# Optimization experiments

Hardware: AMD Instinct MI355X
Metric: run time of the kernel (lower is better)

Reference implementation:

```python
import jax, jax.numpy as jnp
import numpy as np
from math import ceil

B, N, C_IN, H, EDIM = 64, 512, 128, 128, 5
EPG = 16 * N          # edges per graph
E = B * EPG           # 524288 edges total
K1 = ceil(0.5 * N)    # 256 clusters after pool 1
K2 = ceil(0.5 * K1)   # 128 clusters after pool 2
EPS = 1e-15


def dense_mincut_pool(x, adj, s, mask=None):
    # x: [B,n,F], adj: [B,n,n], s: [B,n,k]
    s = jax.nn.softmax(s, axis=-1)
    if mask is not None:
        m = mask[..., None].astype(x.dtype)
        x = x * m
        s = s * m
    out = jnp.einsum('bnk,bnf->bkf', s, x)
    out_adj = jnp.einsum('bnk,bnm,bml->bkl', s, adj, s)
    mincut_num = jnp.trace(out_adj, axis1=-2, axis2=-1)
    d_flat = adj.sum(-1)                                   # degrees [B,n]
    mincut_den = jnp.trace(jnp.einsum('bnk,bn,bnl->bkl', s, d_flat, s), axis1=-2, axis2=-1)
    mincut_loss = jnp.mean(-(mincut_num / mincut_den))
    k = s.shape[-1]
    ss = jnp.einsum('bnk,bnl->bkl', s, s)
    ss_norm = jnp.linalg.norm(ss, axis=(-1, -2), keepdims=True)
    i_s = jnp.eye(k, dtype=x.dtype)
    ortho_loss = jnp.mean(jnp.linalg.norm(ss / ss_norm - i_s / np.sqrt(k), axis=(-1, -2)))
    out_adj = out_adj * (1.0 - i_s)                        # zero diagonal
    d = jnp.sqrt(out_adj.sum(-1))[..., None] + EPS
    out_adj = out_adj / d / jnp.swapaxes(d, -1, -2)
    return out, out_adj, mincut_loss, ortho_loss


def setup_inputs() -> dict:
    key = jax.random.key(0)
    ks = iter(jax.random.split(key, 40))
    NT = B * N
    x = jax.random.normal(next(ks), (NT, C_IN), jnp.float32)
    # within-graph random edges; nodes are sorted by graph (batch = repeat)
    offs = jnp.repeat(jnp.arange(B, dtype=jnp.int32) * N, EPG)
    src = jax.random.randint(next(ks), (E,), 0, N, jnp.int32) + offs
    dst = jax.random.randint(next(ks), (E,), 0, N, jnp.int32) + offs
    edge_index = jnp.stack([src, dst])
    edge_attr = jax.random.normal(next(ks), (E, EDIM), jnp.float32)
    batch = jnp.repeat(jnp.arange(B, dtype=jnp.int32), N)

    def W(shape):
        return jax.random.normal(next(ks), shape, jnp.float32) * 0.05

    inp = dict(x=x, edge_index=edge_index, edge_attr=edge_attr, batch=batch,
               bn_gamma=jnp.ones((C_IN,), jnp.float32), bn_beta=jnp.zeros((C_IN,), jnp.float32),
               Wq=W((C_IN, H)), bq=W((H,)), Wk=W((C_IN, H)), bk=W((H,)),
               Wv=W((C_IN, H)), bv=W((H,)), We=W((EDIM, H)),
               Wskip=W((C_IN, H)), bskip=W((H,)),
               W_mlp1=W((H, K1)), b_mlp1=W((K1,)),
               W2_rel=W((H, H)), b2_rel=W((H,)), W2_root=W((H, H)),
               W_mlp2=W((H, K2)), b_mlp2=W((K2,)),
               W3_rel=W((H, H)), b3_rel=W((H,)), W3_root=W((H, H)),
               W_lin1=W((H, H)), b_lin1=W((H,)),
               W_ro=W((H, 1)), b_ro=W((1,)))
    return inp


def reference(x, edge_index, edge_attr, batch, bn_gamma, bn_beta,
              Wq, bq, Wk, bk, Wv, bv, We, Wskip, bskip,
              W_mlp1, b_mlp1, W2_rel, b2_rel, W2_root,
              W_mlp2, b_mlp2, W3_rel, b3_rel, W3_root,
              W_lin1, b_lin1, W_ro, b_ro):
    NT = x.shape[0]
    # BatchNorm1d (training-mode batch statistics, biased var, eps=1e-5)
    mu = x.mean(0)
    var = x.var(0)
    xh = (x - mu) / jnp.sqrt(var + 1e-5) * bn_gamma + bn_beta

    # TransformerConv (heads=1, concat=True, root_weight=True, edge_dim=5)
    src, dst = edge_index[0], edge_index[1]
    q = xh @ Wq + bq
    k_ = xh @ Wk + bk
    v = xh @ Wv + bv
    e = edge_attr @ We                       # lin_edge has no bias
    kj = k_[src] + e
    vj = v[src] + e
    logits = (q[dst] * kj).sum(-1) / np.sqrt(H)
    m = jax.ops.segment_max(logits, dst, num_segments=NT)
    a = jnp.exp(logits - m[dst])
    denom = jax.ops.segment_sum(a, dst, num_segments=NT)
    alpha = a / denom[dst]
    agg = jax.ops.segment_sum(alpha[:, None] * vj, dst, num_segments=NT)
    h = jax.nn.relu(agg + xh @ Wskip + bskip)

    # to_dense_batch: equal-size graphs sorted by batch -> reshape
    xd = h.reshape(B, N, H)
    mask = jnp.ones((B, N), bool)
    # to_dense_adj: scatter-add edge indicators (duplicates accumulate)
    adj = jnp.zeros((B, N, N), jnp.float32).at[batch[src], src % N, dst % N].add(1.0)

    s = xd @ W_mlp1 + b_mlp1
    xd, adj, mc1, o1 = dense_mincut_pool(xd, adj, s, mask)
    # DenseGraphConv: lin_rel(adj @ x) + lin_root(x)
    xd = jax.nn.relu((adj @ xd) @ W2_rel + b2_rel + xd @ W2_root)
    s = xd @ W_mlp2 + b_mlp2
    xd, adj, mc2, o2 = dense_mincut_pool(xd, adj, s)
    xd = (adj @ xd) @ W3_rel + b3_rel + xd @ W3_root
    g = xd.mean(1)
    g = jax.nn.relu(g @ W_lin1 + b_lin1)
    return jax.nn.sigmoid(g @ W_ro + b_ro).squeeze(-1)   # [B]
```

## Files before the change

### kernel.cpp

```cpp
#include <hip/hip_runtime.h>
#include <math.h>

#define BGRAPH 64
#define NNODE  512
#define NTOT   32768
#define CIN    128
#define HDIM   128
#define EDIM_  5
#define EDGES  524288
#define K1C    256
#define K2C    128

using f32x4 = __attribute__((ext_vector_type(4))) float;
using s16x8 = __attribute__((ext_vector_type(8))) short;

__device__ __forceinline__ short f2bf(float f) {
    union { float f; unsigned u; } v; v.f = f;
    unsigned r = v.u + 0x7fffu + ((v.u >> 16) & 1u);
    return (short)(r >> 16);
}
__device__ __forceinline__ float bf2f(short s) {
    union { unsigned u; float f; } v; v.u = ((unsigned)(unsigned short)s) << 16;
    return v.f;
}

__global__ __launch_bounds__(256) void prep_kernel(const float* __restrict__ x,
                                                   float* __restrict__ psum,
                                                   float* __restrict__ psq,
                                                   const float* __restrict__ Wq, const float* __restrict__ Wk,
                                                   const float* __restrict__ Wv, const float* __restrict__ Ws,
                                                   const float* __restrict__ bq, const float* __restrict__ bk,
                                                   const float* __restrict__ bv, const float* __restrict__ bs,
                                                   float* __restrict__ W4, float* __restrict__ bias4,
                                                   const int* __restrict__ ei,
                                                   int* __restrict__ deg_src,
                                                   int* __restrict__ deg_dst) {
    __shared__ float ss[128], sq[128];
    int tid = threadIdx.x, bid = blockIdx.x;
    if (bid < 256) {
        long idx0 = (long)bid * 256 + tid;
        float4 s = {0.f, 0.f, 0.f, 0.f}, q = {0.f, 0.f, 0.f, 0.f};
#pragma unroll
        for (int it = 0; it < 16; ++it) {
            float4 v = *(const float4*)(x + (idx0 + (long)it * 65536) * 4);
            s.x += v.x; s.y += v.y; s.z += v.z; s.w += v.w;
            q.x += v.x * v.x; q.y += v.y * v.y; q.z += v.z * v.z; q.w += v.w * v.w;
        }
        if (tid < 128) { ss[tid] = 0.f; sq[tid] = 0.f; }
        __syncthreads();
        int c0 = (tid & 31) * 4;
        atomicAdd(&ss[c0 + 0], s.x); atomicAdd(&ss[c0 + 1], s.y);
        atomicAdd(&ss[c0 + 2], s.z); atomicAdd(&ss[c0 + 3], s.w);
        atomicAdd(&sq[c0 + 0], q.x); atomicAdd(&sq[c0 + 1], q.y);
        atomicAdd(&sq[c0 + 2], q.z); atomicAdd(&sq[c0 + 3], q.w);
        __syncthreads();
        if (tid < 128) {
            psum[bid * 128 + tid] = ss[tid];
            psq[bid * 128 + tid]  = sq[tid];
        }
    } else if (bid < 512) {
        int i = (bid - 256) * 256 + tid;
        if (i < 128 * 512) {
            int k = i / 512, j = i % 512;
            float v;
            if (j < 128)      v = Wq[k * 128 + j];
            else if (j < 256) v = Wk[k * 128 + (j - 128)];
            else if (j < 384) v = Wv[k * 128 + (j - 256)];
            else              v = Ws[k * 128 + (j - 384)];
            W4[i] = v;
        }
        if (i < 512) {
            float v;
            if (i < 128)      v = bq[i];
            else if (i < 256) v = bk[i - 128];
            else if (i < 384) v = bv[i - 256];
            else              v = bs[i - 384];
            bias4[i] = v;
        }
    } else {
        int e = (bid - 512) * 256 + tid;
        if (e < EDGES) {
            atomicAdd(&deg_src[ei[e]], 1);
            atomicAdd(&deg_dst[ei[EDGES + e]], 1);
        }
    }
}

__global__ __launch_bounds__(1024) void scan2fin_kernel(const int* __restrict__ deg_src,
                                                        int* __restrict__ rp_src, int* __restrict__ cur_src,
                                                        const int* __restrict__ deg_dst,
                                                        int* __restrict__ rp_dst, int* __restrict__ cur_dst,
                                                        const float* __restrict__ psum,
                                                        const float* __restrict__ psq,
                                                        const float* __restrict__ gamma,
                                                        const float* __restrict__ beta,
                                                        float* __restrict__ scale,
                                                        float* __restrict__ shift) {
    __shared__ int part[1024];
    int tid = threadIdx.x;
    if (blockIdx.x == 2) {
        if (tid < 128) {
            int c = tid;
            float s = 0.f, q = 0.f;
            for (int b = 0; b < 256; ++b) { s += psum[b * 128 + c]; q += psq[b * 128 + c]; }
            float mu  = s / (float)NTOT;
            float var = q / (float)NTOT - mu * mu;
            float rstd = rsqrtf(var + 1e-5f);
            float sc = gamma[c] * rstd;
            scale[c] = sc;
            shift[c] = beta[c] - mu * sc;
        }
        return;
    }
    const int* deg = blockIdx.x ? deg_dst : deg_src;
    int* rowptr    = blockIdx.x ? rp_dst  : rp_src;
    int* cursor    = blockIdx.x ? cur_dst : cur_src;
    int base = tid * 32;
    int s = 0;
    for (int i = 0; i < 32; ++i) s += deg[base + i];
    part[tid] = s;
    __syncthreads();
    for (int off = 1; off < 1024; off <<= 1) {
        int v = part[tid];
        int add = (tid >= off) ? part[tid - off] : 0;
        __syncthreads();
        part[tid] = v + add;
        __syncthreads();
    }
    int run = (tid == 0) ? 0 : part[tid - 1];
    for (int i = 0; i < 32; ++i) {
        rowptr[base + i] = run;
        cursor[base + i] = run;
        run += deg[base + i];
    }
}

__global__ __launch_bounds__(256) void scatter_kernel(const int* __restrict__ ei,
                                                      int* __restrict__ cur_src, int* __restrict__ cur_dst,
                                                      int* __restrict__ eid_src, int* __restrict__ eid_dst) {
    int e = blockIdx.x * 256 + threadIdx.x;
    if (e < EDGES) {
        int s = ei[e], d = ei[EDGES + e];
        eid_src[atomicAdd(&cur_src[s], 1)] = e;
        eid_dst[atomicAdd(&cur_dst[d], 1)] = e;
    }
}

template <int TILE, bool TRANS_A, bool AFFINE, bool ANORM, bool ROWSUM, bool RELU,
          bool DUAL, bool OBF16, bool AU8, bool BBF16, bool ATRBF16, bool ABF16>
__global__ __launch_bounds__(256) void mgemm(const void* __restrict__ Av,
                                             const void* __restrict__ Bv,
                                             const void* __restrict__ A2v,
                                             const void* __restrict__ B2v,
                                             int Ksplit,
                                             const float* __restrict__ bias,
                                             void* __restrict__ Cv,
                                             const float* __restrict__ scale,
                                             const float* __restrict__ shift,
                                             int M, int Nc, int K,
                                             int lda, int ldb, int ldc,
                                             long sA, long sB, long sC) {
    __shared__ __align__(16) short As[TILE * 40];
    __shared__ __align__(16) short Bs[TILE * 40];
    __shared__ float dvl[ANORM ? 256 : 1];
    constexpr int ASZ = AU8 ? 1 : ((ATRBF16 || ABF16) ? 2 : 4);
    constexpr int BSZ = BBF16 ? 2 : 4;
    const char* Abase = (const char*)Av + (long)blockIdx.z * sA * ASZ;
    const char* Bbase = (const char*)Bv + (long)blockIdx.z * sB * BSZ;
    float* C = (float*)Cv + (OBF16 ? 0 : (long)blockIdx.z * sC);
    short* Cs = (short*)Cv + (OBF16 ? (long)blockIdx.z * sC : 0);
    const int m0 = blockIdx.y * TILE, n0 = blockIdx.x * TILE;
    const int tid = threadIdx.x;
    const int lane16 = tid & 15;
    const int quad = (tid & 63) >> 4;
    const int wrow = (tid >> 6) >> 1, wcol = (tid >> 6) & 1;
    constexpr int WT = TILE / 32;

    if (ANORM) {
        for (int i = tid; i < K; i += 256)
            dvl[i] = 1.f / (sqrtf(scale[(long)blockIdx.z * lda + i]) + 1e-15f);
        __syncthreads();
    }

    f32x4 acc[WT][WT] = {};

    for (int k0 = 0; k0 < K; k0 += 32) {
        const char* Au = Abase; const char* Bu = Bbase; int ku = k0;
        if (DUAL && k0 >= Ksplit) { Au = (const char*)A2v; Bu = (const char*)B2v; ku = k0 - Ksplit; }

        if (!TRANS_A) {
#pragma unroll
            for (int p = 0; p < TILE / 32; ++p) {
                int idx = tid + p * 256;
                int row = idx >> 3, c4 = idx & 7;
                short4 o;
                if (AU8) {
                    unsigned u = *(const unsigned*)((const unsigned char*)Au +
                                                    (long)(m0 + row) * lda + ku + c4 * 4);
                    o = make_short4(f2bf((float)(u & 255u)), f2bf((float)((u >> 8) & 255u)),
                                    f2bf((float)((u >> 16) & 255u)), f2bf((float)((u >> 24) & 255u)));
                } else if (ABF16) {
                    o = *(const short4*)((const short*)Au + (long)(m0 + row) * lda + ku + c4 * 4);
                } else {
                    float4 v = *(const float4*)((const float*)Au + (long)(m0 + row) * lda + ku + c4 * 4);
                    if (AFFINE) {
                        int k = ku + c4 * 4;
                        v.x = v.x * scale[k] + shift[k];
                        v.y = v.y * scale[k + 1] + shift[k + 1];
                        v.z = v.z * scale[k + 2] + shift[k + 2];
                        v.w = v.w * scale[k + 3] + shift[k + 3];
                    }
                    if (ANORM) {
                        int k = ku + c4 * 4;
                        int grow = m0 + row;
                        float dr = dvl[grow];
                        v.x = (grow == k + 0) ? 0.f : v.x * dr * dvl[k + 0];
                        v.y = (grow == k + 1) ? 0.f : v.y * dr * dvl[k + 1];
                        v.z = (grow == k + 2) ? 0.f : v.z * dr * dvl[k + 2];
                        v.w = (grow == k + 3) ? 0.f : v.w * dr * dvl[k + 3];
                    }
                    o = make_short4(f2bf(v.x), f2bf(v.y), f2bf(v.z), f2bf(v.w));
                }
                *(short4*)&As[row * 40 + c4 * 4] = o;
            }
        } else {
            if (TILE == 128 || tid < 128) {
                int c4 = tid >> 3, g = tid & 7;
                short* d = &As[(c4 * 4) * 40 + g * 4];
                if (ATRBF16) {
                    const short* src = (const short*)Au + (long)(ku + g * 4) * lda + m0 + c4 * 4;
                    short4 r0 = *(const short4*)(src);
                    short4 r1 = *(const short4*)(src + lda);
                    short4 r2 = *(const short4*)(src + 2 * lda);
                    short4 r3 = *(const short4*)(src + 3 * lda);
                    *(short4*)(d + 0 * 40) = make_short4(r0.x, r1.x, r2.x, r3.x);
                    *(short4*)(d + 1 * 40) = make_short4(r0.y, r1.y, r2.y, r3.y);
                    *(short4*)(d + 2 * 40) = make_short4(r0.z, r1.z, r2.z, r3.z);
                    *(short4*)(d + 3 * 40) = make_short4(r0.w, r1.w, r2.w, r3.w);
                } else {
                    const float* src = (const float*)Au + (long)(ku + g * 4) * lda + m0 + c4 * 4;
                    float4 r0 = *(const float4*)(src);
                    float4 r1 = *(const float4*)(src + lda);
                    float4 r2 = *(const float4*)(src + 2 * lda);
                    float4 r3 = *(const float4*)(src + 3 * lda);
                    *(short4*)(d + 0 * 40) = make_short4(f2bf(r0.x), f2bf(r1.x), f2bf(r2.x), f2bf(r3.x));
                    *(short4*)(d + 1 * 40) = make_short4(f2bf(r0.y), f2bf(r1.y), f2bf(r2.y), f2bf(r3.y));
                    *(short4*)(d + 2 * 40) = make_short4(f2bf(r0.z), f2bf(r1.z), f2bf(r2.z), f2bf(r3.z));
                    *(short4*)(d + 3 * 40) = make_short4(f2bf(r0.w), f2bf(r1.w), f2bf(r2.w), f2bf(r3.w));
                }
            }
        }
        if (TILE == 128 || tid < 128) {
            int c4 = tid >> 3, g = tid & 7;
            short* d = &Bs[(c4 * 4) * 40 + g * 4];
            if (BBF16) {
                const short* src = (const short*)Bu + (long)(ku + g * 4) * ldb + n0 + c4 * 4;
                short4 r0 = *(const short4*)(src);
                short4 r1 = *(const short4*)(src + ldb);
                short4 r2 = *(const short4*)(src + 2 * ldb);
                short4 r3 = *(const short4*)(src + 3 * ldb);
                *(short4*)(d + 0 * 40) = make_short4(r0.x, r1.x, r2.x, r3.x);
                *(short4*)(d + 1 * 40) = make_short4(r0.y, r1.y, r2.y, r3.y);
                *(short4*)(d + 2 * 40) = make_short4(r0.z, r1.z, r2.z, r3.z);
                *(short4*)(d + 3 * 40) = make_short4(r0.w, r1.w, r2.w, r3.w);
            } else {
                const float* src = (const float*)Bu + (long)(ku + g * 4) * ldb + n0 + c4 * 4;
                float4 r0 = *(const float4*)(src);
                float4 r1 = *(const float4*)(src + ldb);
                float4 r2 = *(const float4*)(src + 2 * ldb);
                float4 r3 = *(const float4*)(src + 3 * ldb);
                *(short4*)(d + 0 * 40) = make_short4(f2bf(r0.x), f2bf(r1.x), f2bf(r2.x), f2bf(r3.x));
                *(short4*)(d + 1 * 40) = make_short4(f2bf(r0.y), f2bf(r1.y), f2bf(r2.y), f2bf(r3.y));
                *(short4*)(d + 2 * 40) = make_short4(f2bf(r0.z), f2bf(r1.z), f2bf(r2.z), f2bf(r3.z));
                *(short4*)(d + 3 * 40) = make_short4(f2bf(r0.w), f2bf(r1.w), f2bf(r2.w), f2bf(r3.w));
            }
        }
        __syncthreads();

        s16x8 af[WT], bf[WT];
#pragma unroll
        for (int t = 0; t < WT; ++t) {
            af[t] = *(const s16x8*)&As[(wrow * (TILE / 2) + t * 16 + lane16) * 40 + quad * 8];
            bf[t] = *(const s16x8*)&Bs[(wcol * (TILE / 2) + t * 16 + lane16) * 40 + quad * 8];
        }
#pragma unroll
        for (int i = 0; i < WT; ++i)
#pragma unroll
            for (int j = 0; j < WT; ++j)
                acc[i][j] = __builtin_amdgcn_mfma_f32_16x16x32_bf16(af[i], bf[j], acc[i][j], 0, 0, 0);
        __syncthreads();
    }

#pragma unroll
    for (int i = 0; i < WT; ++i) {
        int gm = m0 + wrow * (TILE / 2) + i * 16 + quad * 4;
#pragma unroll
        for (int j = 0; j < WT; ++j) {
            int gn = n0 + wcol * (TILE / 2) + j * 16 + lane16;
            float bv = bias ? bias[gn] : 0.f;
#pragma unroll
            for (int r = 0; r < 4; ++r) {
                float val = acc[i][j][r] + bv;
                if (RELU) val = fmaxf(val, 0.f);
                if (OBF16) Cs[(long)(gm + r) * ldc + gn] = f2bf(val);
                else       C[(long)(gm + r) * ldc + gn] = val;
            }
        }
    }

    if (ROWSUM) {
        float* rlA = (float*)As;
        float* rlB = (float*)Bs;
#pragma unroll
        for (int i = 0; i < WT; ++i) {
#pragma unroll
            for (int r = 0; r < 4; ++r) {
                int gm = m0 + wrow * (TILE / 2) + i * 16 + quad * 4 + r;
                float p = 0.f;
#pragma unroll
                for (int j = 0; j < WT; ++j) {
                    int gn = n0 + wcol * (TILE / 2) + j * 16 + lane16;
                    p += (gn == gm) ? 0.f : acc[i][j][r];
                }
#pragma unroll
                for (int off = 1; off < 16; off <<= 1) p += __shfl_xor(p, off);
                if (lane16 == 0) {
                    int rl = wrow * (TILE / 2) + i * 16 + quad * 4 + r;
                    (wcol ? rlB : rlA)[rl] = p;
                }
            }
        }
        __syncthreads();
        float* rout = (float*)shift;
        for (int t = tid; t < TILE; t += 256)
            atomicAdd(&rout[(long)blockIdx.z * M + m0 + t], rlA[t] + rlB[t]);
    }
}

template <int KADJ, bool RELU, bool OBF16>
__global__ __launch_bounds__(256) void fused_gc_kernel(const float* __restrict__ adj,
                                                       const float* __restrict__ rowsum,
                                                       const float* __restrict__ xp,
                                                       const float* __restrict__ Wrel,
                                                       const float* __restrict__ brel,
                                                       const float* __restrict__ Wroot,
                                                       void* __restrict__ Outv) {
    __shared__ __align__(16) short As[64 * 40];
    __shared__ __align__(16) short Bs[128 * 40];
    __shared__ __align__(16) short Tl[64][136];
    __shared__ float dvl[KADJ];
    const int z = blockIdx.y;
    const int m0 = blockIdx.x * 64;
    const int tid = threadIdx.x;
    const int lane16 = tid & 15;
    const int quad = (tid & 63) >> 4;
    const int wrow = (tid >> 6) >> 1, wcol = (tid >> 6) & 1;
    const float* adjz = adj + (long)z * KADJ * KADJ;
    const float* xpz  = xp + (long)z * KADJ * 128;

    for (int i = tid; i < KADJ; i += 256)
        dvl[i] = 1.f / (sqrtf(rowsum[(long)z * KADJ + i]) + 1e-15f);
    __syncthreads();

    f32x4 acc[2][4] = {};
    for (int k0 = 0; k0 < KADJ; k0 += 32) {
#pragma unroll
        for (int p = 0; p < 2; ++p) {
            int idx = tid + p * 256;
            int row = idx >> 3, c4 = idx & 7;
            int grow = m0 + row, k = k0 + c4 * 4;
            float4 v = *(const float4*)(adjz + (long)grow * KADJ + k);
            float dr = dvl[grow];
            v.x = (grow == k + 0) ? 0.f : v.x * dr * dvl[k + 0];
            v.y = (grow == k + 1) ? 0.f : v.y * dr * dvl[k + 1];
            v.z = (grow == k + 2) ? 0.f : v.z * dr * dvl[k + 2];
            v.w = (grow == k + 3) ? 0.f : v.w * dr * dvl[k + 3];
            *(short4*)&As[row * 40 + c4 * 4] =
                make_short4(f2bf(v.x), f2bf(v.y), f2bf(v.z), f2bf(v.w));
        }
        {
            int c4 = tid >> 3, g = tid & 7;
            short* d = &Bs[(c4 * 4) * 40 + g * 4];
            const float* src = xpz + (long)(k0 + g * 4) * 128 + c4 * 4;
            float4 r0 = *(const float4*)(src);
            float4 r1 = *(const float4*)(src + 128);
            float4 r2 = *(const float4*)(src + 256);
            float4 r3 = *(const float4*)(src + 384);
            *(short4*)(d + 0 * 40) = make_short4(f2bf(r0.x), f2bf(r1.x), f2bf(r2.x), f2bf(r3.x));
            *(short4*)(d + 1 * 40) = make_short4(f2bf(r0.y), f2bf(r1.y), f2bf(r2.y), f2bf(r3.y));
            *(short4*)(d + 2 * 40) = make_short4(f2bf(r0.z), f2bf(r1.z), f2bf(r2.z), f2bf(r3.z));
            *(short4*)(d + 3 * 40) = make_short4(f2bf(r0.w), f2bf(r1.w), f2bf(r2.w), f2bf(r3.w));
        }
        __syncthreads();
        s16x8 af[2], bf[4];
#pragma unroll
        for (int t = 0; t < 2; ++t)
            af[t] = *(const s16x8*)&As[(wrow * 32 + t * 16 + lane16) * 40 + quad * 8];
#pragma unroll
        for (int j = 0; j < 4; ++j)
            bf[j] = *(const s16x8*)&Bs[(wcol * 64 + j * 16 + lane16) * 40 + quad * 8];
#pragma unroll
        for (int t = 0; t < 2; ++t)
#pragma unroll
            for (int j = 0; j < 4; ++j)
                acc[t][j] = __builtin_amdgcn_mfma_f32_16x16x32_bf16(af[t], bf[j], acc[t][j], 0, 0, 0);
        __syncthreads();
    }
#pragma unroll
    for (int t = 0; t < 2; ++t)
#pragma unroll
        for (int j = 0; j < 4; ++j)
#pragma unroll
            for (int r = 0; r < 4; ++r)
                Tl[wrow * 32 + t * 16 + quad * 4 + r][wcol * 64 + j * 16 + lane16] =
                    f2bf(acc[t][j][r]);
    __syncthreads();

    f32x4 acc2[2][4] = {};
    for (int k0 = 0; k0 < 256; k0 += 32) {
        const bool useXp = (k0 >= 128);
        const float* Wsrc = useXp ? (Wroot + (long)(k0 - 128) * 128)
                                  : (Wrel + (long)k0 * 128);
        {
            int c4 = tid >> 3, g = tid & 7;
            short* d = &Bs[(c4 * 4) * 40 + g * 4];
            const float* src = Wsrc + (long)(g * 4) * 128 + c4 * 4;
            float4 r0 = *(const float4*)(src);
            float4 r1 = *(const float4*)(src + 128);
            float4 r2 = *(const float4*)(src + 256);
            float4 r3 = *(const float4*)(src + 384);
            *(short4*)(d + 0 * 40) = make_short4(f2bf(r0.x), f2bf(r1.x), f2bf(r2.x), f2bf(r3.x));
            *(short4*)(d + 1 * 40) = make_short4(f2bf(r0.y), f2bf(r1.y), f2bf(r2.y), f2bf(r3.y));
            *(short4*)(d + 2 * 40) = make_short4(f2bf(r0.z), f2bf(r1.z), f2bf(r2.z), f2bf(r3.z));
            *(short4*)(d + 3 * 40) = make_short4(f2bf(r0.w), f2bf(r1.w), f2bf(r2.w), f2bf(r3.w));
        }
        if (useXp) {
#pragma unroll
            for (int p = 0; p < 2; ++p) {
                int idx = tid + p * 256;
                int row = idx >> 3, c4 = idx & 7;
                float4 v = *(const float4*)(xpz + (long)(m0 + row) * 128 + (k0 - 128) + c4 * 4);
                *(short4*)&As[row * 40 + c4 * 4] =
                    make_short4(f2bf(v.x), f2bf(v.y), f2bf(v.z), f2bf(v.w));
            }
        }
        __syncthreads();
        s16x8 af[2], bf[4];
#pragma unroll
        for (int t = 0; t < 2; ++t) {
            int ar = wrow * 32 + t * 16 + lane16;
            af[t] = useXp ? *(const s16x8*)&As[ar * 40 + quad * 8]
                          : *(const s16x8*)&Tl[ar][k0 + quad * 8];
        }
#pragma unroll
        for (int j = 0; j < 4; ++j)
            bf[j] = *(const s16x8*)&Bs[(wcol * 64 + j * 16 + lane16) * 40 + quad * 8];
#pragma unroll
        for (int t = 0; t < 2; ++t)
#pragma unroll
            for (int j = 0; j < 4; ++j)
                acc2[t][j] = __builtin_amdgcn_mfma_f32_16x16x32_bf16(af[t], bf[j], acc2[t][j], 0, 0, 0);
        __syncthreads();
    }

    float* Of = (float*)Outv;
    short* Ob = (short*)Outv;
#pragma unroll
    for (int t = 0; t < 2; ++t) {
#pragma unroll
        for (int j = 0; j < 4; ++j) {
            int gcol = wcol * 64 + j * 16 + lane16;
            float bv = brel[gcol];
#pragma unroll
            for (int r = 0; r < 4; ++r) {
                int grow = m0 + wrow * 32 + t * 16 + quad * 4 + r;
                float val = acc2[t][j][r] + bv;
                if (RELU) val = fmaxf(val, 0.f);
                long oi = ((long)z * KADJ + grow) * 128 + gcol;
                if (OBF16) Ob[oi] = f2bf(val);
                else       Of[oi] = val;
            }
        }
    }
}

template <int NC>
__global__ __launch_bounds__(256) void mlp_softmax_kernel(const short* __restrict__ A,
                                                          const float* __restrict__ W,
                                                          const float* __restrict__ bias,
                                                          short* __restrict__ Out) {
    __shared__ __align__(16) short As[64 * 40];
    __shared__ __align__(16) short Ws[NC * 40];
    const int tid = threadIdx.x;
    const int lane16 = tid & 15;
    const int quad = (tid & 63) >> 4;
    const int wv = tid >> 6;
    const int m0 = blockIdx.x * 64;
    constexpr int NT = NC / 16;

    f32x4 acc[NT] = {};

    for (int k0 = 0; k0 < 128; k0 += 32) {
        {
            int row = tid >> 2, g = tid & 3;
            *(s16x8*)&As[row * 40 + g * 8] =
                *(const s16x8*)(A + (long)(m0 + row) * 128 + k0 + g * 8);
        }
#pragma unroll
        for (int p = 0; p < NC / 128; ++p) {
            int c4 = tid >> 3, g = tid & 7;
            int n0 = p * 128 + c4 * 4;
            short* d = &Ws[n0 * 40 + g * 4];
            const float* src = W + (long)(k0 + g * 4) * NC + n0;
            float4 r0 = *(const float4*)(src);
            float4 r1 = *(const float4*)(src + NC);
            float4 r2 = *(const float4*)(src + 2 * NC);
            float4 r3 = *(const float4*)(src + 3 * NC);
            *(short4*)(d + 0 * 40) = make_short4(f2bf(r0.x), f2bf(r1.x), f2bf(r2.x), f2bf(r3.x));
            *(short4*)(d + 1 * 40) = make_short4(f2bf(r0.y), f2bf(r1.y), f2bf(r2.y), f2bf(r3.y));
            *(short4*)(d + 2 * 40) = make_short4(f2bf(r0.z), f2bf(r1.z), f2bf(r2.z), f2bf(r3.z));
            *(short4*)(d + 3 * 40) = make_short4(f2bf(r0.w), f2bf(r1.w), f2bf(r2.w), f2bf(r3.w));
        }
        __syncthreads();

        s16x8 af = *(const s16x8*)&As[(wv * 16 + lane16) * 40 + quad * 8];
#pragma unroll
        for (int t = 0; t < NT; ++t) {
            s16x8 bf = *(const s16x8*)&Ws[(t * 16 + lane16) * 40 + quad * 8];
            acc[t] = __builtin_amdgcn_mfma_f32_16x16x32_bf16(af, bf, acc[t], 0, 0, 0);
        }
        __syncthreads();
    }

    float mx[4] = {-INFINITY, -INFINITY, -INFINITY, -INFINITY};
#pragma unroll
    for (int t = 0; t < NT; ++t) {
        float bv = bias[t * 16 + lane16];
#pragma unroll
        for (int r = 0; r < 4; ++r) {
            float x = bf2f(f2bf(acc[t][r] + bv));
            acc[t][r] = x;
            mx[r] = fmaxf(mx[r], x);
        }
    }
#pragma unroll
    for (int off = 8; off; off >>= 1)
#pragma unroll
        for (int r = 0; r < 4; ++r) mx[r] = fmaxf(mx[r], __shfl_xor(mx[r], off));
    float sm[4] = {0.f, 0.f, 0.f, 0.f};
#pragma unroll
    for (int t = 0; t < NT; ++t)
#pragma unroll
        for (int r = 0; r < 4; ++r) {
            float e = expf(acc[t][r] - mx[r]);
            acc[t][r] = e;
            sm[r] += e;
        }
#pragma unroll
    for (int off = 8; off; off >>= 1)
#pragma unroll
        for (int r = 0; r < 4; ++r) sm[r] += __shfl_xor(sm[r], off);
#pragma unroll
    for (int r = 0; r < 4; ++r) sm[r] = 1.f / sm[r];
#pragma unroll
    for (int t = 0; t < NT; ++t)
#pragma unroll
        for (int r = 0; r < 4; ++r)
            Out[(long)(m0 + wv * 16 + quad * 4 + r) * NC + t * 16 + lane16] =
                f2bf(acc[t][r] * sm[r]);
}

template <bool OBF16>
__global__ __launch_bounds__(256) void bgemm(const short* __restrict__ A,
                                             const short* __restrict__ B,
                                             void* __restrict__ Cv,
                                             float outscale,
                                             int M, int Nc, int K,
                                             int lda, int ldb, int ldc,
                                             long sA, long sB, long sC) {
    __shared__ __align__(16) short As[128 * 40];
    __shared__ __align__(16) short Bs[128 * 40];
    int L = blockIdx.x + (blockIdx.y << 2) + (blockIdx.z << 4);
    int xcd = L & 7, i = L >> 3;
    const int z = xcd * 8 + (i >> 4);
    const int m0 = ((i >> 2) & 3) * 128, n0 = (i & 3) * 128;
    A += (long)z * sA;
    B += (long)z * sB;
    float* C = (float*)Cv + (OBF16 ? 0 : (long)z * sC);
    short* Cs = (short*)Cv + (OBF16 ? (long)z * sC : 0);
    const int tid = threadIdx.x;
    const int lane16 = tid & 15;
    const int quad = (tid & 63) >> 4;
    const int wrow = (tid >> 6) >> 1, wcol = (tid >> 6) & 1;

    f32x4 acc[4][4] = {};

    for (int k0 = 0; k0 < K; k0 += 32) {
#pragma unroll
        for (int p = 0; p < 2; ++p) {
            int u = tid + p * 256;
            int row = u >> 2, g = u & 3;
            *(s16x8*)&As[row * 40 + g * 8] =
                *(const s16x8*)(A + (long)(m0 + row) * lda + k0 + g * 8);
        }
#pragma unroll
        for (int p = 0; p < 2; ++p) {
            int u = tid + p * 256;
            int row = u >> 2, g = u & 3;
            *(s16x8*)&Bs[row * 40 + g * 8] =
                *(const s16x8*)(B + (long)(n0 + row) * ldb + k0 + g * 8);
        }
        __syncthreads();

        s16x8 af[4], bf[4];
#pragma unroll
        for (int t = 0; t < 4; ++t) {
            af[t] = *(const s16x8*)&As[(wrow * 64 + t * 16 + lane16) * 40 + quad * 8];
            bf[t] = *(const s16x8*)&Bs[(wcol * 64 + t * 16 + lane16) * 40 + quad * 8];
        }
#pragma unroll
        for (int i2 = 0; i2 < 4; ++i2)
#pragma unroll
            for (int j = 0; j < 4; ++j)
                acc[i2][j] = __builtin_amdgcn_mfma_f32_16x16x32_bf16(af[i2], bf[j], acc[i2][j], 0, 0, 0);
        __syncthreads();
    }

#pragma unroll
    for (int i2 = 0; i2 < 4; ++i2) {
        int gm = m0 + wrow * 64 + i2 * 16 + quad * 4;
#pragma unroll
        for (int j = 0; j < 4; ++j) {
            int gn = n0 + wcol * 64 + j * 16 + lane16;
#pragma unroll
            for (int r = 0; r < 4; ++r) {
                float val = acc[i2][j][r] * outscale;
                if (OBF16) Cs[(long)(gm + r) * ldc + gn] = f2bf(val);
                else       C[(long)(gm + r) * ldc + gn] = val;
            }
        }
    }
}

__global__ __launch_bounds__(256) void attn_pv_kernel(const short* __restrict__ S,
                                                      const int* __restrict__ ei,
                                                      const float* __restrict__ eattr,
                                                      const float* __restrict__ We,
                                                      const int* __restrict__ rp_dst,
                                                      const int* __restrict__ deg_dst,
                                                      const int* __restrict__ eid_dst,
                                                      const short* __restrict__ qkvs,
                                                      float* __restrict__ alpha,
                                                      short* __restrict__ h) {
    __shared__ float sWe[EDIM_ * 128];
    __shared__ __align__(16) short sS[16][528];
    int g = threadIdx.x >> 4;
    int lane = threadIdx.x & 15;
    int gbase = (threadIdx.x & 63) & ~15;
    int b = blockIdx.x;
    int xcd = b & 7, idx = b >> 3;
    int nb = (xcd * 8 + (idx >> 5)) * 32 + (idx & 31);
    int node = nb * 16 + g;

    {
        const short* Srow = S + (long)node * 512;
        short* Sl = sS[g];
#pragma unroll
        for (int j = 0; j < 4; ++j)
            *(s16x8*)&Sl[j * 128 + lane * 8] = *(const s16x8*)(Srow + j * 128 + lane * 8);
    }
    for (int i = threadIdx.x; i < EDIM_ * 128; i += 256) sWe[i] = We[i];
    __syncthreads();
    const short* Sl = sS[g];

    float qw[EDIM_];
    {
        s16x8 qv = *(const s16x8*)(qkvs + (long)node * 512 + lane * 8);
        float qf[8];
#pragma unroll
        for (int j = 0; j < 8; ++j) qf[j] = bf2f(qv[j]);
#pragma unroll
        for (int d = 0; d < EDIM_; ++d) {
            float p = 0.f;
#pragma unroll
            for (int j = 0; j < 8; ++j) p += qf[j] * sWe[d * 128 + lane * 8 + j];
            qw[d] = p;
        }
#pragma unroll
        for (int off = 8; off; off >>= 1)
#pragma unroll
            for (int d = 0; d < EDIM_; ++d) qw[d] += __shfl_xor(qw[d], off);
#pragma unroll
        for (int d = 0; d < EDIM_; ++d) qw[d] *= 0.08838834764831845f;
    }

    int start = rp_dst[node], cnt = deg_dst[node];
    int nch = (cnt + 15) >> 4;

    float lsum = 0.f, a5[EDIM_] = {};
    int   src_c[4] = {0, 0, 0, 0};
    float a_c[4]   = {0.f, 0.f, 0.f, 0.f};
    for (int c = 0; c < nch; ++c) {
        int t = c * 16 + lane;
        int src = 0; float wv = 0.f;
        if (t < cnt) {
            int e = eid_dst[start + t];
            src = ei[e];
            float lg = bf2f(Sl[src & 511]);
            float ea[EDIM_];
#pragma unroll
            for (int d = 0; d < EDIM_; ++d) { ea[d] = eattr[e * EDIM_ + d]; lg += ea[d] * qw[d]; }
            wv = expf(lg);
            lsum += wv;
#pragma unroll
            for (int d = 0; d < EDIM_; ++d) a5[d] += wv * ea[d];
        }
        if (c < 4) { src_c[c] = src; a_c[c] = wv; }
        else if (t < cnt) alpha[start + t] = wv;
    }
#pragma unroll
    for (int off = 8; off; off >>= 1) {
        lsum += __shfl_xor(lsum, off);
#pragma unroll
        for (int d = 0; d < EDIM_; ++d) a5[d] += __shfl_xor(a5[d], off);
    }
    float inv = (lsum > 0.f) ? 1.f / lsum : 0.f;
    float e5[EDIM_];
#pragma unroll
    for (int d = 0; d < EDIM_; ++d) e5[d] = a5[d] * inv;

    float acc[8] = {};
    for (int c = 0; c < nch; ++c) {
        int src; float a;
        if (c < 4) { src = src_c[c]; a = a_c[c]; }
        else {
            int t = c * 16 + lane;
            if (t < cnt) {
                int e = eid_dst[start + t];
                src = ei[e];
                a = alpha[start + t];
            } else { src = 0; a = 0.f; }
        }
        int m = min(16, cnt - c * 16);
        if (m == 16) {
#pragma unroll
            for (int j = 0; j < 16; ++j) {
                int   sj = __shfl(src, gbase + j);
                float aj = __shfl(a,   gbase + j);
                s16x8 v = *(const s16x8*)(qkvs + (long)sj * 512 + 256 + lane * 8);
#pragma unroll
                for (int k = 0; k < 8; ++k) acc[k] += aj * bf2f(v[k]);
            }
        } else {
            for (int j = 0; j < m; ++j) {
                int   sj = __shfl(src, gbase + j);
                float aj = __shfl(a,   gbase + j);
                s16x8 v = *(const s16x8*)(qkvs + (long)sj * 512 + 256 + lane * 8);
#pragma unroll
                for (int k = 0; k < 8; ++k) acc[k] += aj * bf2f(v[k]);
            }
        }
    }

    s16x8 sk = *(const s16x8*)(qkvs + (long)node * 512 + 384 + lane * 8);
    s16x8 o;
#pragma unroll
    for (int j = 0; j < 8; ++j) {
        float ec = 0.f;
#pragma unroll
        for (int d = 0; d < EDIM_; ++d) ec += e5[d] * sWe[d * 128 + lane * 8 + j];
        float val = acc[j] * inv + ec + bf2f(sk[j]);
        o[j] = f2bf(fmaxf(val, 0.f));
    }
    *(s16x8*)(h + (long)node * 128 + lane * 8) = o;
}

__global__ __launch_bounds__(256) void t1_gather_kernel(const int* __restrict__ ei,
                                                        const int* __restrict__ rp_src,
                                                        const int* __restrict__ deg_src,
                                                        const int* __restrict__ eid_src,
                                                        const short* __restrict__ s1b,
                                                        short* __restrict__ T1s) {
    int g = threadIdx.x >> 4;
    int lane = threadIdx.x & 15;
    int gbase = (threadIdx.x & 63) & ~15;
    int b = blockIdx.x;
    int xcd = b & 7, idx = b >> 3;
    int nb = (xcd * 8 + (idx >> 5)) * 32 + (idx & 31);
    int node = nb * 16 + g;

    int start = rp_src[node], cnt = deg_src[node];
    int nch = (cnt + 15) >> 4;
    float acc[16] = {};
    for (int c = 0; c < nch; ++c) {
        int t = c * 16 + lane;
        int dst = 0;
        if (t < cnt) {
            int e = eid_src[start + t];
            dst = ei[EDGES + e];
        }
        int m = min(16, cnt - c * 16);
        if (m == 16) {
#pragma unroll
            for (int j = 0; j < 16; ++j) {
                int dj = __shfl(dst, gbase + j);
                const s16x8* p = (const s16x8*)(s1b + (long)dj * 256 + lane * 16);
                s16x8 v0 = p[0], v1 = p[1];
#pragma unroll
                for (int k = 0; k < 8; ++k) { acc[k] += bf2f(v0[k]); acc[8 + k] += bf2f(v1[k]); }
            }
        } else {
            for (int j = 0; j < m; ++j) {
                int dj = __shfl(dst, gbase + j);
                const s16x8* p = (const s16x8*)(s1b + (long)dj * 256 + lane * 16);
                s16x8 v0 = p[0], v1 = p[1];
#pragma unroll
                for (int k = 0; k < 8; ++k) { acc[k] += bf2f(v0[k]); acc[8 + k] += bf2f(v1[k]); }
            }
        }
    }
    s16x8 o0, o1;
#pragma unroll
    for (int k = 0; k < 8; ++k) { o0[k] = f2bf(acc[k]); o1[k] = f2bf(acc[8 + k]); }
    short* o = T1s + (long)node * 256 + lane * 16;
    *(s16x8*)(o)     = o0;
    *(s16x8*)(o + 8) = o1;
}

__global__ __launch_bounds__(128) void readout_kernel(const float* __restrict__ xd3,
                                                      const float* __restrict__ W_lin1,
                                                      const float* __restrict__ b_lin1,
                                                      const float* __restrict__ W_ro,
                                                      const float* __restrict__ b_ro,
                                                      float* __restrict__ out) {
    int b = blockIdx.x, t = threadIdx.x;
    __shared__ float g[128], g2[128], wred[2];
    const float* X = xd3 + (long)b * K2C * 128;
    float s = 0.f;
    for (int r = 0; r < K2C; ++r) s += X[r * 128 + t];
    g[t] = s * (1.f / (float)K2C);
    __syncthreads();
    float u = b_lin1[t];
    for (int k = 0; k < 128; ++k) u += g[k] * W_lin1[k * 128 + t];
    g2[t] = fmaxf(u, 0.f);
    __syncthreads();
    float p = g2[t] * W_ro[t];
#pragma unroll
    for (int off = 32; off; off >>= 1) p += __shfl_xor(p, off);
    if ((t & 63) == 0) wred[t >> 6] = p;
    __syncthreads();
    if (t == 0) {
        float tot = wred[0] + wred[1] + b_ro[0];
        out[b] = 1.f / (1.f + expf(-tot));
    }
}

extern "C" void kernel_launch(void* const* d_in, const int* in_sizes, int n_in,
                              void* d_out, int out_size, void* d_ws, size_t ws_size,
                              hipStream_t stream) {
    const float* x      = (const float*)d_in[0];
    const int*   ei     = (const int*)d_in[1];
    const float* eattr  = (const float*)d_in[2];
    const float* gamma  = (const float*)d_in[4];
    const float* beta   = (const float*)d_in[5];
    const float* Wq     = (const float*)d_in[6];
    const float* bq     = (const float*)d_in[7];
    const float* Wk     = (const float*)d_in[8];
    const float* bk     = (const float*)d_in[9];
    const float* Wv     = (const float*)d_in[10];
    const float* bv     = (const float*)d_in[11];
    const float* We     = (const float*)d_in[12];
    const float* Wskip  = (const float*)d_in[13];
    const float* bskip  = (const float*)d_in[14];
    const float* W_mlp1 = (const float*)d_in[15];
    const float* b_mlp1 = (const float*)d_in[16];
    const float* W2_rel = (const float*)d_in[17];
    const float* b2_rel = (const float*)d_in[18];
    const float* W2_root= (const float*)d_in[19];
    const float* W_mlp2 = (const float*)d_in[20];
    const float* b_mlp2 = (const float*)d_in[21];
    const float* W3_rel = (const float*)d_in[22];
    const float* b3_rel = (const float*)d_in[23];
    const float* W3_root= (const float*)d_in[24];
    const float* W_lin1 = (const float*)d_in[25];
    const float* b_lin1 = (const float*)d_in[26];
    const float* W_ro   = (const float*)d_in[27];
    const float* b_ro   = (const float*)d_in[28];
    float* out = (float*)d_out;

    char* w = (char*)d_ws;
    const size_t MB = 1ull << 20;
    short* qkvs = (short*)(w + 0);
    short* S    = (short*)(w + 32 * MB);
    short* T1s  = (short*)(w + 48 * MB);
    short* s1b  = (short*)(w + 64 * MB);
    short* xd2  = (short*)(w + 56 * MB);
    short* s2b  = (short*)(w + 72 * MB);
    float* t2   = (float*)(w + 64 * MB);
    float* adj2 = (float*)(w + 0);
    float* xp2  = (float*)(w + 4 * MB);
    float* xd3  = (float*)(w + 12 * MB);
    short* h    = (short*)(w + 80 * MB);
    float* adj1 = (float*)(w + 80 * MB);
    float* xp1  = (float*)(w + 96 * MB);
    float* alpha= (float*)(w + 97 * MB);
    char* misc  = w + 104 * MB;
    float* W4     = (float*)(misc + 0x00000);
    float* bias4  = (float*)(misc + 0x40000);
    float* scale  = (float*)(misc + 0x41400);
    float* shift  = (float*)(misc + 0x41600);
    float* rowsum1= (float*)(misc + 0x42000);
    float* rowsum2= (float*)(misc + 0x52000);
    int* deg_src  = (int*)(misc + 0x60000);
    int* deg_dst  = (int*)(misc + 0x80000);
    int* rp_src   = (int*)(misc + 0xA0000);
    int* rp_dst   = (int*)(misc + 0xC0000);
    int* cur_src  = (int*)(misc + 0xE0000);
    int* cur_dst  = (int*)(misc + 0x100000);
    int* eid_src  = (int*)(misc + 0x120000);
    int* eid_dst  = (int*)(misc + 0x320000);
    float* psum   = (float*)(misc + 0x520000);
    float* psq    = (float*)(misc + 0x540000);

    hipMemsetAsync(misc + 0x42000, 0, 0xA0000 - 0x42000, stream);

    prep_kernel<<<2560, 256, 0, stream>>>(x, psum, psq,
                                          Wq, Wk, Wv, Wskip, bq, bk, bv, bskip,
                                          W4, bias4, ei, deg_src, deg_dst);

    scan2fin_kernel<<<3, 1024, 0, stream>>>(deg_src, rp_src, cur_src,
                                            deg_dst, rp_dst, cur_dst,
                                            psum, psq, gamma, beta, scale, shift);

    scatter_kernel<<<EDGES / 256, 256, 0, stream>>>(ei, cur_src, cur_dst, eid_src, eid_dst);

    mgemm<128, false, true, false, false, false, false, true, false, false, false, false>
        <<<dim3(4, 256, 1), 256, 0, stream>>>(
        x, W4, nullptr, nullptr, 0, bias4, qkvs, scale, shift,
        NTOT, 512, 128, 128, 512, 512, 0, 0, 0);

    bgemm<true><<<dim3(4, 4, BGRAPH), 256, 0, stream>>>(
        qkvs + 0, qkvs + 128, S, 0.08838834764831845f,
        NNODE, NNODE, 128, 512, 512, 512,
        (long)NNODE * 512, (long)NNODE * 512, (long)NNODE * NNODE);

    attn_pv_kernel<<<NTOT / 16, 256, 0, stream>>>(
        S, ei, eattr, We, rp_dst, deg_dst, eid_dst, qkvs, alpha, h);

    mlp_softmax_kernel<K1C><<<NTOT / 64, 256, 0, stream>>>(h, W_mlp1, b_mlp1, s1b);

    t1_gather_kernel<<<NTOT / 16, 256, 0, stream>>>(
        ei, rp_src, deg_src, eid_src, s1b, T1s);

    mgemm<64, true, false, false, false, false, false, false, false, true, true, false>
        <<<dim3(2, 4, BGRAPH), 256, 0, stream>>>(
        s1b, h, nullptr, nullptr, 0, nullptr, xp1, nullptr, nullptr,
        K1C, 128, NNODE, K1C, 128, 128,
        (long)NNODE * K1C, (long)NNODE * 128, (long)K1C * 128);
    mgemm<128, true, false, false, true, false, false, false, false, true, true, false>
        <<<dim3(2, 2, BGRAPH), 256, 0, stream>>>(
        s1b, T1s, nullptr, nullptr, 0, nullptr, adj1, nullptr, rowsum1,
        K1C, K1C, NNODE, K1C, K1C, K1C,
        (long)NNODE * K1C, (long)NNODE * K1C, (long)K1C * K1C);

    fused_gc_kernel<K1C, true, true><<<dim3(4, BGRAPH), 256, 0, stream>>>(
        adj1, rowsum1, xp1, W2_rel, b2_rel, W2_root, xd2);

    mlp_softmax_kernel<K2C><<<(BGRAPH * K1C) / 64, 256, 0, stream>>>(xd2, W_mlp2, b_mlp2, s2b);

    mgemm<64, false, false, true, false, false, false, false, false, true, false, false>
        <<<dim3(2, 4, BGRAPH), 256, 0, stream>>>(
        adj1, s2b, nullptr, nullptr, 0, nullptr, t2, rowsum1, nullptr,
        K1C, K2C, K1C, K1C, K2C, K2C,
        (long)K1C * K1C, (long)K1C * K2C, (long)K1C * K2C);
    mgemm<64, true, false, false, true, false, false, false, false, false, true, false>
        <<<dim3(2, 2, BGRAPH), 256, 0, stream>>>(
        s2b, t2, nullptr, nullptr, 0, nullptr, adj2, nullptr, rowsum2,
        K2C, K2C, K1C, K2C, K2C, K2C,
        (long)K1C * K2C, (long)K1C * K2C, (long)K2C * K2C);
    mgemm<64, true, false, false, false, false, false, false, false, true, true, false>
        <<<dim3(2, 2, BGRAPH), 256, 0, stream>>>(
        s2b, xd2, nullptr, nullptr, 0, nullptr, xp2, nullptr, nullptr,
        K2C, 128, K1C, K2C, 128, 128,
        (long)K1C * K2C, (long)K1C * 128, (long)K2C * 128);

    fused_gc_kernel<K2C, false, false><<<dim3(2, BGRAPH), 256, 0, stream>>>(
        adj2, rowsum2, xp2, W3_rel, b3_rel, W3_root, xd3);

    readout_kernel<<<BGRAPH, 128, 0, stream>>>(xd3, W_lin1, b_lin1, W_ro, b_ro, out);

    (void)in_sizes; (void)n_in; (void)out_size; (void)ws_size;
}
```

Baseline: 482.2 us.

## Merge independent GEMM launches and fuse final graph-conv column sum into readout

Refactors mgemm into a device body so several independent GEMMs (and the edge scatter) can run as one launch: the QKVS projection with the CSR scatter, the two pool-1 GEMMs, and two of the pool-2 GEMMs. The last graph-conv kernel now accumulates per-graph column sums through shared and global atomics instead of writing xd3, and the readout reads those sums directly. The goal is to cut launch count and serialization gaps and to drop one intermediate buffer. In exchange it adds atomics and heterogeneous blocks within a launch, and the h buffer is moved to a new workspace offset.

```diff
diff --git a/kernel.cpp b/kernel.cpp
--- a/kernel.cpp
+++ b/kernel.cpp
@@ -95,7 +95,8 @@
                                                         const float* __restrict__ gamma,
                                                         const float* __restrict__ beta,
                                                         float* __restrict__ scale,
-                                                        float* __restrict__ shift) {
+                                                        float* __restrict__ shift,
+                                                        float* __restrict__ gsum) {
     __shared__ int part[1024];
     int tid = threadIdx.x;
     if (blockIdx.x == 2) {
@@ -110,6 +111,7 @@
             scale[c] = sc;
             shift[c] = beta[c] - mu * sc;
         }
+        for (int i = tid; i < BGRAPH * 128; i += 1024) gsum[i] = 0.f;
         return;
     }
     const int* deg = blockIdx.x ? deg_dst : deg_src;
@@ -135,41 +137,29 @@
     }
 }
 
-__global__ __launch_bounds__(256) void scatter_kernel(const int* __restrict__ ei,
-                                                      int* __restrict__ cur_src, int* __restrict__ cur_dst,
-                                                      int* __restrict__ eid_src, int* __restrict__ eid_dst) {
-    int e = blockIdx.x * 256 + threadIdx.x;
-    if (e < EDGES) {
-        int s = ei[e], d = ei[EDGES + e];
-        eid_src[atomicAdd(&cur_src[s], 1)] = e;
-        eid_dst[atomicAdd(&cur_dst[d], 1)] = e;
-    }
-}
-
 template <int TILE, bool TRANS_A, bool AFFINE, bool ANORM, bool ROWSUM, bool RELU,
           bool DUAL, bool OBF16, bool AU8, bool BBF16, bool ATRBF16, bool ABF16>
-__global__ __launch_bounds__(256) void mgemm(const void* __restrict__ Av,
-                                             const void* __restrict__ Bv,
-                                             const void* __restrict__ A2v,
-                                             const void* __restrict__ B2v,
-                                             int Ksplit,
-                                             const float* __restrict__ bias,
-                                             void* __restrict__ Cv,
-                                             const float* __restrict__ scale,
-                                             const float* __restrict__ shift,
-                                             int M, int Nc, int K,
-                                             int lda, int ldb, int ldc,
-                                             long sA, long sB, long sC) {
-    __shared__ __align__(16) short As[TILE * 40];
-    __shared__ __align__(16) short Bs[TILE * 40];
-    __shared__ float dvl[ANORM ? 256 : 1];
+__device__ __forceinline__ void mgemm_body(short* As, short* Bs, float* dvl,
+                                           const void* __restrict__ Av,
+                                           const void* __restrict__ Bv,
+                                           const void* __restrict__ A2v,
+                                           const void* __restrict__ B2v,
+                                           int Ksplit,
+                                           const float* __restrict__ bias,
+                                           void* __restrict__ Cv,
+                                           const float* __restrict__ scale,
+                                           const float* __restrict__ shift,
+                                           int M, int Nc, int K,
+                                           int lda, int ldb, int ldc,
+                                           long sA, long sB, long sC,
+                                           int bx, int by, int bz) {
     constexpr int ASZ = AU8 ? 1 : ((ATRBF16 || ABF16) ? 2 : 4);
     constexpr int BSZ = BBF16 ? 2 : 4;
-    const char* Abase = (const char*)Av + (long)blockIdx.z * sA * ASZ;
-    const char* Bbase = (const char*)Bv + (long)blockIdx.z * sB * BSZ;
-    float* C = (float*)Cv + (OBF16 ? 0 : (long)blockIdx.z * sC);
-    short* Cs = (short*)Cv + (OBF16 ? (long)blockIdx.z * sC : 0);
-    const int m0 = blockIdx.y * TILE, n0 = blockIdx.x * TILE;
+    const char* Abase = (const char*)Av + (long)bz * sA * ASZ;
+    const char* Bbase = (const char*)Bv + (long)bz * sB * BSZ;
+    float* C = (float*)Cv + (OBF16 ? 0 : (long)bz * sC);
+    short* Cs = (short*)Cv + (OBF16 ? (long)bz * sC : 0);
+    const int m0 = by * TILE, n0 = bx * TILE;
     const int tid = threadIdx.x;
     const int lane16 = tid & 15;
     const int quad = (tid & 63) >> 4;
@@ -178,7 +168,7 @@
 
     if (ANORM) {
         for (int i = tid; i < K; i += 256)
-            dvl[i] = 1.f / (sqrtf(scale[(long)blockIdx.z * lda + i]) + 1e-15f);
+            dvl[i] = 1.f / (sqrtf(scale[(long)bz * lda + i]) + 1e-15f);
         __syncthreads();
     }
 
@@ -333,11 +323,114 @@
         __syncthreads();
         float* rout = (float*)shift;
         for (int t = tid; t < TILE; t += 256)
-            atomicAdd(&rout[(long)blockIdx.z * M + m0 + t], rlA[t] + rlB[t]);
-    }
-}
-
-template <int KADJ, bool RELU, bool OBF16>
+            atomicAdd(&rout[(long)bz * M + m0 + t], rlA[t] + rlB[t]);
+    }
+}
+
+template <int TILE, bool TRANS_A, bool AFFINE, bool ANORM, bool ROWSUM, bool RELU,
+          bool DUAL, bool OBF16, bool AU8, bool BBF16, bool ATRBF16, bool ABF16>
+__global__ __launch_bounds__(256) void mgemm(const void* __restrict__ Av,
+                                             const void* __restrict__ Bv,
+                                             const void* __restrict__ A2v,
+                                             const void* __restrict__ B2v,
+                                             int Ksplit,
+                                             const float* __restrict__ bias,
+                                             void* __restrict__ Cv,
+                                             const float* __restrict__ scale,
+                                             const float* __restrict__ shift,
+                                             int M, int Nc, int K,
+                                             int lda, int ldb, int ldc,
+                                             long sA, long sB, long sC) {
+    __shared__ __align__(16) short As[TILE * 40];
+    __shared__ __align__(16) short Bs[TILE * 40];
+    __shared__ float dvl[ANORM ? 256 : 1];
+    mgemm_body<TILE, TRANS_A, AFFINE, ANORM, ROWSUM, RELU, DUAL, OBF16, AU8, BBF16, ATRBF16, ABF16>(
+        As, Bs, dvl, Av, Bv, A2v, B2v, Ksplit, bias, Cv, scale, shift,
+        M, Nc, K, lda, ldb, ldc, sA, sB, sC,
+        blockIdx.x, blockIdx.y, blockIdx.z);
+}
+
+__global__ __launch_bounds__(256) void qkvs_scatter_kernel(const float* __restrict__ x,
+                                                           const float* __restrict__ W4,
+                                                           const float* __restrict__ bias4,
+                                                           short* __restrict__ qkvs,
+                                                           const float* __restrict__ scale,
+                                                           const float* __restrict__ shift,
+                                                           const int* __restrict__ ei,
+                                                           int* __restrict__ cur_src,
+                                                           int* __restrict__ cur_dst,
+                                                           int* __restrict__ eid_src,
+                                                           int* __restrict__ eid_dst) {
+    __shared__ __align__(16) short As[128 * 40];
+    __shared__ __align__(16) short Bs[128 * 40];
+    int b = blockIdx.x;
+    if (b < 1024) {
+        mgemm_body<128, false, true, false, false, false, false, true, false, false, false, false>(
+            As, Bs, nullptr, x, W4, nullptr, nullptr, 0, bias4, qkvs, scale, shift,
+            NTOT, 512, 128, 128, 512, 512, 0, 0, 0,
+            b & 3, b >> 2, 0);
+    } else {
+        int e = (b - 1024) * 256 + threadIdx.x;
+        if (e < EDGES) {
+            int s = ei[e], d = ei[EDGES + e];
+            eid_src[atomicAdd(&cur_src[s], 1)] = e;
+            eid_dst[atomicAdd(&cur_dst[d], 1)] = e;
+        }
+    }
+}
+
+__global__ __launch_bounds__(256) void pool1_kernel(const short* __restrict__ s1b,
+                                                    const short* __restrict__ h,
+                                                    const short* __restrict__ T1s,
+                                                    float* __restrict__ xp1,
+                                                    float* __restrict__ adj1,
+                                                    float* __restrict__ rowsum1) {
+    __shared__ __align__(16) short As[128 * 40];
+    __shared__ __align__(16) short Bs[128 * 40];
+    int b = blockIdx.x;
+    if (b < 512) {
+        mgemm_body<64, true, false, false, false, false, false, false, false, true, true, false>(
+            As, Bs, nullptr, s1b, h, nullptr, nullptr, 0, nullptr, xp1, nullptr, nullptr,
+            K1C, 128, NNODE, K1C, 128, 128,
+            (long)NNODE * K1C, (long)NNODE * 128, (long)K1C * 128,
+            b & 1, (b >> 1) & 3, b >> 3);
+    } else {
+        int j = b - 512;
+        mgemm_body<128, true, false, false, true, false, false, false, false, true, true, false>(
+            As, Bs, nullptr, s1b, T1s, nullptr, nullptr, 0, nullptr, adj1, nullptr, rowsum1,
+            K1C, K1C, NNODE, K1C, K1C, K1C,
+            (long)NNODE * K1C, (long)NNODE * K1C, (long)K1C * K1C,
+            j & 1, (j >> 1) & 1, j >> 2);
+    }
+}
+
+__global__ __launch_bounds__(256) void pool2_kernel(const float* __restrict__ adj1,
+                                                    const float* __restrict__ rowsum1,
+                                                    const short* __restrict__ s2b,
+                                                    const short* __restrict__ xd2,
+                                                    float* __restrict__ t2,
+                                                    float* __restrict__ xp2) {
+    __shared__ __align__(16) short As[64 * 40];
+    __shared__ __align__(16) short Bs[64 * 40];
+    __shared__ float dvl[256];
+    int b = blockIdx.x;
+    if (b < 512) {
+        mgemm_body<64, false, false, true, false, false, false, false, false, true, false, false>(
+            As, Bs, dvl, adj1, s2b, nullptr, nullptr, 0, nullptr, t2, rowsum1, nullptr,
+            K1C, K2C, K1C, K1C, K2C, K2C,
+            (long)K1C * K1C, (long)K1C * K2C, (long)K1C * K2C,
+            b & 1, (b >> 1) & 3, b >> 3);
+    } else {
+        int j = b - 512;
+        mgemm_body<64, true, false, false, false, false, false, false, false, true, true, false>(
+            As, Bs, nullptr, s2b, xd2, nullptr, nullptr, 0, nullptr, xp2, nullptr, nullptr,
+            K2C, 128, K1C, K2C, 128, 128,
+            (long)K1C * K2C, (long)K1C * 128, (long)K2C * 128,
+            j & 1, (j >> 1) & 1, j >> 2);
+    }
+}
+
+template <int KADJ, bool RELU, bool OBF16, bool COLSUM>
 __global__ __launch_bounds__(256) void fused_gc_kernel(const float* __restrict__ adj,
                                                        const float* __restrict__ rowsum,
                                                        const float* __restrict__ xp,
@@ -349,6 +442,7 @@
     __shared__ __align__(16) short Bs[128 * 40];
     __shared__ __align__(16) short Tl[64][136];
     __shared__ float dvl[KADJ];
+    __shared__ float cs[COLSUM ? 128 : 1];
     const int z = blockIdx.y;
     const int m0 = blockIdx.x * 64;
     const int tid = threadIdx.x;
@@ -360,6 +454,7 @@
 
     for (int i = tid; i < KADJ; i += 256)
         dvl[i] = 1.f / (sqrtf(rowsum[(long)z * KADJ + i]) + 1e-15f);
+    if (COLSUM) for (int i = tid; i < 128; i += 256) cs[i] = 0.f;
     __syncthreads();
 
     f32x4 acc[2][4] = {};
@@ -463,24 +558,46 @@
         __syncthreads();
     }
 
-    float* Of = (float*)Outv;
-    short* Ob = (short*)Outv;
-#pragma unroll
-    for (int t = 0; t < 2; ++t) {
+    if (!COLSUM) {
+        float* Of = (float*)Outv;
+        short* Ob = (short*)Outv;
+#pragma unroll
+        for (int t = 0; t < 2; ++t) {
+#pragma unroll
+            for (int j = 0; j < 4; ++j) {
+                int gcol = wcol * 64 + j * 16 + lane16;
+                float bv = brel[gcol];
+#pragma unroll
+                for (int r = 0; r < 4; ++r) {
+                    int grow = m0 + wrow * 32 + t * 16 + quad * 4 + r;
+                    float val = acc2[t][j][r] + bv;
+                    if (RELU) val = fmaxf(val, 0.f);
+                    long oi = ((long)z * KADJ + grow) * 128 + gcol;
+                    if (OBF16) Ob[oi] = f2bf(val);
+                    else       Of[oi] = val;
+                }
+            }
+        }
+    } else {
 #pragma unroll
         for (int j = 0; j < 4; ++j) {
             int gcol = wcol * 64 + j * 16 + lane16;
             float bv = brel[gcol];
-#pragma unroll
-            for (int r = 0; r < 4; ++r) {
-                int grow = m0 + wrow * 32 + t * 16 + quad * 4 + r;
-                float val = acc2[t][j][r] + bv;
-                if (RELU) val = fmaxf(val, 0.f);
-                long oi = ((long)z * KADJ + grow) * 128 + gcol;
-                if (OBF16) Ob[oi] = f2bf(val);
-                else       Of[oi] = val;
-            }
-        }
+            float p = 0.f;
+#pragma unroll
+            for (int t = 0; t < 2; ++t)
+#pragma unroll
+                for (int r = 0; r < 4; ++r) {
+                    float val = acc2[t][j][r] + bv;
+                    if (RELU) val = fmaxf(val, 0.f);
+                    p += val;
+                }
+            atomicAdd(&cs[gcol], p);
+        }
+        __syncthreads();
+        float* gsum = (float*)Outv;
+        for (int i = tid; i < 128; i += 256)
+            atomicAdd(&gsum[(long)z * 128 + i], cs[i]);
     }
 }
 
@@ -827,7 +944,7 @@
     *(s16x8*)(o + 8) = o1;
 }
 
-__global__ __launch_bounds__(128) void readout_kernel(const float* __restrict__ xd3,
+__global__ __launch_bounds__(128) void readout_kernel(const float* __restrict__ gsum,
                                                       const float* __restrict__ W_lin1,
                                                       const float* __restrict__ b_lin1,
                                                       const float* __restrict__ W_ro,
@@ -835,10 +952,7 @@
                                                       float* __restrict__ out) {
     int b = blockIdx.x, t = threadIdx.x;
     __shared__ float g[128], g2[128], wred[2];
-    const float* X = xd3 + (long)b * K2C * 128;
-    float s = 0.f;
-    for (int r = 0; r < K2C; ++r) s += X[r * 128 + t];
-    g[t] = s * (1.f / (float)K2C);
+    g[t] = gsum[(long)b * 128 + t] * (1.f / (float)K2C);
     __syncthreads();
     float u = b_lin1[t];
     for (int k = 0; k < 128; ++k) u += g[k] * W_lin1[k * 128 + t];
@@ -899,11 +1013,10 @@
     float* t2   = (float*)(w + 64 * MB);
     float* adj2 = (float*)(w + 0);
     float* xp2  = (float*)(w + 4 * MB);
-    float* xd3  = (float*)(w + 12 * MB);
-    short* h    = (short*)(w + 80 * MB);
     float* adj1 = (float*)(w + 80 * MB);
     float* xp1  = (float*)(w + 96 * MB);
     float* alpha= (float*)(w + 97 * MB);
+    short* h    = (short*)(w + 112 * MB);
     char* misc  = w + 104 * MB;
     float* W4     = (float*)(misc + 0x00000);
     float* bias4  = (float*)(misc + 0x40000);
@@ -921,6 +1034,7 @@
     int* eid_dst  = (int*)(misc + 0x320000);
     float* psum   = (float*)(misc + 0x520000);
     float* psq    = (float*)(misc + 0x540000);
+    float* gsum   = (float*)(misc + 0x560000);
 
     hipMemsetAsync(misc + 0x42000, 0, 0xA0000 - 0x42000, stream);
 
@@ -930,14 +1044,10 @@
 
     scan2fin_kernel<<<3, 1024, 0, stream>>>(deg_src, rp_src, cur_src,
                                             deg_dst, rp_dst, cur_dst,
-                                            psum, psq, gamma, beta, scale, shift);
-
-    scatter_kernel<<<EDGES / 256, 256, 0, stream>>>(ei, cur_src, cur_dst, eid_src, eid_dst);
-
-    mgemm<128, false, true, false, false, false, false, true, false, false, false, false>
-        <<<dim3(4, 256, 1), 256, 0, stream>>>(
-        x, W4, nullptr, nullptr, 0, bias4, qkvs, scale, shift,
-        NTOT, 512, 128, 128, 512, 512, 0, 0, 0);
+                                            psum, psq, gamma, beta, scale, shift, gsum);
+
+    qkvs_scatter_kernel<<<3072, 256, 0, stream>>>(x, W4, bias4, qkvs, scale, shift,
+                                                  ei, cur_src, cur_dst, eid_src, eid_dst);
 
     bgemm<true><<<dim3(4, 4, BGRAPH), 256, 0, stream>>>(
         qkvs + 0, qkvs + 128, S, 0.08838834764831845f,
@@ -952,42 +1062,25 @@
     t1_gather_kernel<<<NTOT / 16, 256, 0, stream>>>(
         ei, rp_src, deg_src, eid_src, s1b, T1s);
 
-    mgemm<64, true, false, false, false, false, false, false, false, true, true, false>
-        <<<dim3(2, 4, BGRAPH), 256, 0, stream>>>(
-        s1b, h, nullptr, nullptr, 0, nullptr, xp1, nullptr, nullptr,
-        K1C, 128, NNODE, K1C, 128, 128,
-        (long)NNODE * K1C, (long)NNODE * 128, (long)K1C * 128);
-    mgemm<128, true, false, false, true, false, false, false, false, true, true, false>
-        <<<dim3(2, 2, BGRAPH), 256, 0, stream>>>(
-        s1b, T1s, nullptr, nullptr, 0, nullptr, adj1, nullptr, rowsum1,
-        K1C, K1C, NNODE, K1C, K1C, K1C,
-        (long)NNODE * K1C, (long)NNODE * K1C, (long)K1C * K1C);
-
-    fused_gc_kernel<K1C, true, true><<<dim3(4, BGRAPH), 256, 0, stream>>>(
+    pool1_kernel<<<768, 256, 0, stream>>>(s1b, h, T1s, xp1, adj1, rowsum1);
+
+    fused_gc_kernel<K1C, true, true, false><<<dim3(4, BGRAPH), 256, 0, stream>>>(
         adj1, rowsum1, xp1, W2_rel, b2_rel, W2_root, xd2);
 
     mlp_softmax_kernel<K2C><<<(BGRAPH * K1C) / 64, 256, 0, stream>>>(xd2, W_mlp2, b_mlp2, s2b);
 
-    mgemm<64, false, false, true, false, false, false, false, false, true, false, false>
-        <<<dim3(2, 4, BGRAPH), 256, 0, stream>>>(
-        adj1, s2b, nullptr, nullptr, 0, nullptr, t2, rowsum1, nullptr,
-        K1C, K2C, K1C, K1C, K2C, K2C,
-        (long)K1C * K1C, (long)K1C * K2C, (long)K1C * K2C);
+    pool2_kernel<<<768, 256, 0, stream>>>(adj1, rowsum1, s2b, xd2, t2, xp2);
+
     mgemm<64, true, false, false, true, false, false, false, false, false, true, false>
         <<<dim3(2, 2, BGRAPH), 256, 0, stream>>>(
         s2b, t2, nullptr, nullptr, 0, nullptr, adj2, nullptr, rowsum2,
         K2C, K2C, K1C, K2C, K2C, K2C,
         (long)K1C * K2C, (long)K1C * K2C, (long)K2C * K2C);
-    mgemm<64, true, false, false, false, false, false, false, false, true, true, false>
-        <<<dim3(2, 2, BGRAPH), 256, 0, stream>>>(
-        s2b, xd2, nullptr, nullptr, 0, nullptr, xp2, nullptr, nullptr,
-        K2C, 128, K1C, K2C, 128, 128,
-        (long)K1C * K2C, (long)K1C * 128, (long)K2C * 128);
-
-    fused_gc_kernel<K2C, false, false><<<dim3(2, BGRAPH), 256, 0, stream>>>(
-        adj2, rowsum2, xp2, W3_rel, b3_rel, W3_root, xd3);
-
-    readout_kernel<<<BGRAPH, 128, 0, stream>>>(xd3, W_lin1, b_lin1, W_ro, b_ro, out);
+
+    fused_gc_kernel<K2C, false, false, true><<<dim3(2, BGRAPH), 256, 0, stream>>>(
+        adj2, rowsum2, xp2, W3_rel, b3_rel, W3_root, gsum);
+
+    readout_kernel<<<BGRAPH, 128, 0, stream>>>(gsum, W_lin1, b_lin1, W_ro, b_ro, out);
 
     (void)in_sizes; (void)n_in; (void)out_size; (void)ws_size;
 }
```

Result: faster. 444.5 us (-7.8%).
